# Kernel optimization log

Measured on AMD Instinct MI355X. Metric: run time of the kernel, lower is better.

Reference implementation:

```python
import jax, jax.numpy as jnp
import numpy as np
import math

C = 256
N_HEAD = 8
GROUPS = 32
EPS = 1e-5


def group_norm(x, scale, bias, groups=GROUPS, eps=EPS):
    # x: [B, C, H, W]
    b, c, h, w = x.shape
    xg = x.reshape(b, groups, c // groups, h, w)
    mean = xg.mean(axis=(2, 3, 4), keepdims=True)
    var = xg.var(axis=(2, 3, 4), keepdims=True)
    xg = (xg - mean) * jax.lax.rsqrt(var + eps)
    x = xg.reshape(b, c, h, w)
    return x * scale[None, :, None, None] + bias[None, :, None, None]


def setup_inputs() -> dict:
    key = jax.random.key(0)
    ks = jax.random.split(key, 8)
    B, H, W = 8, 32, 32
    inp = {
        "input_q": jax.random.normal(ks[0], (B, C, H, W), dtype=jnp.float32),
        "input_kv": jax.random.normal(ks[1], (B, C, H, W), dtype=jnp.float32),
        # GroupNorm affine params (torch default: weight=1, bias=0)
        "gq_scale": jnp.ones((C,), jnp.float32),
        "gq_bias": jnp.zeros((C,), jnp.float32),
        "gkv_scale": jnp.ones((C,), jnp.float32),
        "gkv_bias": jnp.zeros((C,), jnp.float32),
        # 1x1 convs as [out, in] matrices
        "Wq": jax.random.normal(ks[2], (C, C), dtype=jnp.float32) / math.sqrt(C),
        "Wkv": jax.random.normal(ks[3], (2 * C, C), dtype=jnp.float32) / math.sqrt(C),
        "Wout": jax.random.normal(ks[4], (C, C), dtype=jnp.float32) / math.sqrt(C),
        "bout": jnp.zeros((C,), jnp.float32),
    }
    return inp


def reference(input_q, input_kv, gq_scale, gq_bias, gkv_scale, gkv_bias, Wq, Wkv, Wout, bout):
    b, c, h, w = input_q.shape
    n = N_HEAD
    d = c // n

    norm_q = group_norm(input_q, gq_scale, gq_bias)
    query = jnp.einsum('oc,bchw->bohw', Wq, norm_q).reshape(b, n, d, h, w)

    norm_kv = group_norm(input_kv, gkv_scale, gkv_bias)
    kv = jnp.einsum('oc,bchw->bohw', Wkv, norm_kv).reshape(b, n, 2 * d, h, w)
    key, value = kv[:, :, :d], kv[:, :, d:]

    attn = jnp.einsum('bnchw,bncyx->bnhwyx', query, key) / math.sqrt(c)
    attn = jax.nn.softmax(attn.reshape(b, n, h, w, h * w), axis=-1)
    attn = attn.reshape(b, n, h, w, h, w)

    out = jnp.einsum('bnhwyx,bncyx->bnchw', attn, value).reshape(b, c, h, w)
    out = jnp.einsum('oc,bchw->bohw', Wout, out) + bout[None, :, None, None]
    return out + input_q
```

## Files before the change

### kernel.cpp

```cpp
#include <hip/hip_runtime.h>
#include <hip/hip_bf16.h>
#include <math.h>
#include <string.h>

#define NB 8
#define NC 256
#define HWSZ 1024
#define NHEAD 8
#define DHEAD 32
#define NGRP 32
#define CPG 8
#define EPSV 1e-5f

typedef float f32x4 __attribute__((ext_vector_type(4)));
typedef short bf16x8 __attribute__((ext_vector_type(8)));

__device__ __forceinline__ unsigned pk2(float a, float b) {
    __hip_bfloat162 h = __float22bfloat162_rn(make_float2(a, b));
    unsigned r;
    memcpy(&r, &h, sizeof(r));
    return r;
}
__device__ __forceinline__ unsigned pk2t(float a, float b) {
    unsigned ua = __float_as_uint(a), ub = __float_as_uint(b);
    return (ua >> 16) | (ub & 0xFFFF0000u);
}
__device__ __forceinline__ unsigned short f2bf(float x) {
    __hip_bfloat16 h = __float2bfloat16(x);
    unsigned short r;
    memcpy(&r, &h, sizeof(r));
    return r;
}
__device__ __forceinline__ float ex2(float x) { return __builtin_amdgcn_exp2f(x); }

__device__ __forceinline__ void gload_lds16(const void* g, void* l) {
    __builtin_amdgcn_global_load_lds(
        (const __attribute__((address_space(1))) unsigned int*)g,
        (__attribute__((address_space(3))) unsigned int*)l, 16, 0, 0);
}

__global__ void gn_stats_kernel(const float* __restrict__ xq,
                                const float* __restrict__ xkv,
                                float* __restrict__ stats) {
    int idx = blockIdx.x;
    int which = idx >> 8;
    int b = (idx >> 5) & 7;
    int g = idx & 31;
    const float* x = which ? xkv : xq;
    const float4* xb = (const float4*)(x + ((size_t)(b * NC + g * CPG)) * HWSZ);
    float s = 0.f, ss = 0.f;
    for (int i = threadIdx.x; i < (CPG * HWSZ) / 4; i += 256) {
        float4 v = xb[i];
        s += v.x + v.y + v.z + v.w;
        ss += v.x * v.x + v.y * v.y + v.z * v.z + v.w * v.w;
    }
    #pragma unroll
    for (int off = 32; off > 0; off >>= 1) {
        s += __shfl_down(s, off);
        ss += __shfl_down(ss, off);
    }
    __shared__ float red[8];
    int wid = threadIdx.x >> 6;
    if ((threadIdx.x & 63) == 0) { red[wid * 2] = s; red[wid * 2 + 1] = ss; }
    __syncthreads();
    if (threadIdx.x == 0) {
        float S = red[0] + red[2] + red[4] + red[6];
        float SS = red[1] + red[3] + red[5] + red[7];
        float mean = S * (1.f / (CPG * HWSZ));
        float var = SS * (1.f / (CPG * HWSZ)) - mean * mean;
        stats[idx * 2] = mean;
        stats[idx * 2 + 1] = rsqrtf(var + EPSV);
    }
}

__global__ void wconv_kernel(const float* __restrict__ Wq,
                             const float* __restrict__ Wkv,
                             const float* __restrict__ Wout,
                             unsigned short* __restrict__ wqb,
                             unsigned short* __restrict__ wkvb,
                             unsigned short* __restrict__ woutb) {
    int gid = blockIdx.x * 256 + threadIdx.x;
    int i0 = gid * 8;
    const float* src; unsigned short* dst; int off; float sc = 1.f;
    if (i0 < 65536)       { src = Wq;   dst = wqb;   off = i0;          sc = 0.0625f * 1.44269504088896f; }
    else if (i0 < 196608) { src = Wkv;  dst = wkvb;  off = i0 - 65536; }
    else                  { src = Wout; dst = woutb; off = i0 - 196608; }
    float4 v0 = *(const float4*)&src[off];
    float4 v1 = *(const float4*)&src[off + 4];
    uint4 o;
    o.x = pk2(v0.x * sc, v0.y * sc); o.y = pk2(v0.z * sc, v0.w * sc);
    o.z = pk2(v1.x * sc, v1.y * sc); o.w = pk2(v1.z * sc, v1.w * sc);
    *(uint4*)&dst[off] = o;
}

__global__ __launch_bounds__(256) void norm_t_kernel(
        const float* __restrict__ xq, const float* __restrict__ xkv,
        const float* __restrict__ stats,
        const float* __restrict__ sq, const float* __restrict__ bq,
        const float* __restrict__ skv, const float* __restrict__ bkv,
        unsigned short* __restrict__ xnq, unsigned short* __restrict__ xnkv) {
    __shared__ unsigned short T[64][72];
    const int bz = blockIdx.z;
    const int which = bz >> 3, b = bz & 7;
    const int c0 = blockIdx.y * 64, p0 = blockIdx.x * 64;
    const float* x  = which ? xkv : xq;
    const float* sc = which ? skv : sq;
    const float* bi = which ? bkv : bq;
    const float* st = stats + ((size_t)which * 256 + b * 32) * 2;
    const int tid = threadIdx.x;
    const int cb = tid >> 4, pb = tid & 15;
    float mm[4][4];
    #pragma unroll
    for (int u = 0; u < 4; ++u) {
        int c = c0 + cb * 4 + u;
        float4 v = *(const float4*)&x[((size_t)b * NC + c) * HWSZ + p0 + pb * 4];
        int gg = c >> 3;
        float mean = st[gg * 2], rstd = st[gg * 2 + 1];
        float a = rstd * sc[c];
        float bbv = bi[c] - mean * a;
        mm[u][0] = v.x * a + bbv; mm[u][1] = v.y * a + bbv;
        mm[u][2] = v.z * a + bbv; mm[u][3] = v.w * a + bbv;
    }
    #pragma unroll
    for (int v = 0; v < 4; ++v) {
        uint2 s2;
        s2.x = pk2(mm[0][v], mm[1][v]);
        s2.y = pk2(mm[2][v], mm[3][v]);
        *(uint2*)&T[pb * 4 + v][cb * 4] = s2;
    }
    __syncthreads();
    unsigned short* dst = (which ? xnkv : xnq) + (size_t)b * HWSZ * NC;
    #pragma unroll
    for (int it = 0; it < 2; ++it) {
        int i = tid + it * 256;
        int row = i >> 3, seg = i & 7;
        *(uint4*)&dst[(size_t)(p0 + row) * NC + c0 + seg * 8] = *(const uint4*)&T[row][seg * 8];
    }
}

template<int MODE>
__global__ __launch_bounds__(256) void gemm_kernel(
        const unsigned short* __restrict__ Abase,
        const unsigned short* __restrict__ Bbase,
        const float* __restrict__ bias_out,
        const float* __restrict__ resid,
        void* __restrict__ out0, void* __restrict__ out1) {
    __shared__ unsigned short As[64 * 256];
    __shared__ unsigned short Bs[64 * 256];
    const int tid = threadIdx.x;
    const int l16 = tid & 15, g = (tid >> 4) & 3, w = tid >> 6;
    const int o0 = blockIdx.y * 64;
    const size_t prow0 = (size_t)blockIdx.x * 64;
    const unsigned short* Asrc = (MODE < 2) ? (Abase + (size_t)o0 * NC) : (Abase + prow0 * NC);
    const unsigned short* Bsrc = (MODE < 2) ? (Bbase + prow0 * NC) : (Bbase + (size_t)o0 * NC);
    #pragma unroll
    for (int it = 0; it < 8; ++it) {
        int idx = tid + it * 256;
        int row = idx >> 5, seg = idx & 31;
        int ds = row * 256 + ((seg ^ (row & 7)) << 3);
        *(uint4*)&As[ds] = *(const uint4*)&Asrc[(size_t)row * NC + seg * 8];
        *(uint4*)&Bs[ds] = *(const uint4*)&Bsrc[(size_t)row * NC + seg * 8];
    }
    __syncthreads();
    f32x4 acc[4] = {};
    const int abase = (w * 16 + l16) * 256;
    const int asw = l16 & 7;
    #pragma unroll
    for (int kk = 0; kk < 8; ++kk) {
        const int koff = ((kk * 4 + g) ^ asw) << 3;
        bf16x8 a = *(const bf16x8*)&As[abase + koff];
        #pragma unroll
        for (int j = 0; j < 4; ++j) {
            bf16x8 b = *(const bf16x8*)&Bs[(j * 16 + l16) * 256 + koff];
            acc[j] = __builtin_amdgcn_mfma_f32_16x16x32_bf16(a, b, acc[j], 0, 0, 0);
        }
    }
    const int b = (int)(prow0 >> 10);
    const int pp = (int)(prow0 & 1023);
    if (MODE == 0) {
        int ob_ = o0 + 16 * w + 4 * g;
        int n = ob_ >> 5, d0 = ob_ & 31;
        unsigned short* dst = (unsigned short*)out0 + ((size_t)(b * NHEAD + n) * HWSZ) * DHEAD + d0;
        #pragma unroll
        for (int j = 0; j < 4; ++j) {
            int p = pp + 16 * j + l16;
            uint2 st;
            st.x = pk2(acc[j][0], acc[j][1]);
            st.y = pk2(acc[j][2], acc[j][3]);
            *(uint2*)&dst[(size_t)p * DHEAD] = st;
        }
    } else if (MODE == 1) {
        int n = o0 >> 6;
        int d0 = 16 * (w & 1) + 4 * g;
        if (w < 2) {
            unsigned short* dst = (unsigned short*)out0 + ((size_t)(b * NHEAD + n) * HWSZ) * DHEAD + d0;
            #pragma unroll
            for (int j = 0; j < 4; ++j) {
                int p = pp + 16 * j + l16;
                uint2 st;
                st.x = pk2(acc[j][0], acc[j][1]);
                st.y = pk2(acc[j][2], acc[j][3]);
                *(uint2*)&dst[(size_t)p * DHEAD] = st;
            }
        } else {
            unsigned short* dst = (unsigned short*)out1 + ((size_t)(b * NHEAD + n) * DHEAD + d0) * HWSZ;
            #pragma unroll
            for (int j = 0; j < 4; ++j) {
                int slot = ((l16 >> 2) << 3) + ((j & 1) << 2) + (l16 & 3);
                int p = pp + 32 * (j >> 1) + slot;
                #pragma unroll
                for (int r = 0; r < 4; ++r)
                    dst[(size_t)r * HWSZ + p] = f2bf(acc[j][r]);
            }
        }
    } else {
        int p_b = pp + 16 * w + 4 * g;
        #pragma unroll
        for (int j = 0; j < 4; ++j) {
            int o = o0 + 16 * j + l16;
            float bo = bias_out[o];
            size_t off = ((size_t)b * NC + o) * HWSZ + p_b;
            float4 rs = *(const float4*)&resid[off];
            float4 vst = make_float4(acc[j][0] + bo + rs.x, acc[j][1] + bo + rs.y,
                                     acc[j][2] + bo + rs.z, acc[j][3] + bo + rs.w);
            *(float4*)&((float*)out0)[off] = vst;
        }
    }
}

__global__ __launch_bounds__(256) void attn_mfma_kernel(
        const unsigned short* __restrict__ qb,
        const unsigned short* __restrict__ kb,
        const unsigned short* __restrict__ vb,
        unsigned short* __restrict__ ob) {
    __shared__ unsigned short KV[3][4096];
    const int tid = threadIdx.x;
    const int w = tid >> 6, lane = tid & 63;
    const int l16 = lane & 15, g = lane >> 4;
    const int F = blockIdx.y * 16 + blockIdx.x;
    const int bn = (F & 7) * 8 + (F >> 7);
    const int qblk = (F >> 3) & 15;
    const int qp = qblk * 64 + w * 16 + l16;

    bf16x8 qf = *(const bf16x8*)(qb + ((size_t)bn * HWSZ + qp) * DHEAD + g * 8);

    const int kr = tid >> 2, ks = tid & 3;
    const unsigned short* ksrc = kb + (size_t)bn * HWSZ * DHEAD
                               + (size_t)kr * DHEAD + ((ks ^ (kr & 3)) << 3);
    const int vr = tid >> 3, vs = tid & 7;
    const unsigned short* vsrc = vb + (size_t)bn * DHEAD * HWSZ
                               + (size_t)vr * HWSZ + ((vs ^ (vr & 7)) << 3);
    unsigned short* lk = &KV[0][0] + w * 512;
    unsigned short* lv = &KV[0][2048] + w * 512;

#define STAGE(t) do {                                                        \
        int b3_ = (t) % 3; int ti_ = (t) & 15;                               \
        gload_lds16(ksrc + (size_t)ti_ * 64 * DHEAD, lk + b3_ * 4096);       \
        gload_lds16(vsrc + (size_t)ti_ * 64,         lv + b3_ * 4096);       \
    } while (0)

    f32x4 acc0 = {0.f, 0.f, 0.f, 0.f}, acc1 = {0.f, 0.f, 0.f, 0.f};
    float m = -INFINITY, l0 = 0.f, l1 = 0.f;
    const f32x4 z = {0.f, 0.f, 0.f, 0.f};

    const int ksw  = (g ^ (l16 & 3)) << 3;
    const int vsw0 = ((g)     ^ (l16 & 7)) << 3;
    const int vsw1 = ((4 + g) ^ (l16 & 7)) << 3;

    STAGE(0);
    STAGE(1);

    for (int t = 0; t < 16; ++t) {
        const int cur = t % 3;
        asm volatile("s_waitcnt vmcnt(2)" ::: "memory");
        __builtin_amdgcn_s_barrier();
        STAGE(t + 2);

        const unsigned short* Kb = &KV[cur][0];
        const unsigned short* Vb = &KV[cur][2048];
        bf16x8 ka0 = *(const bf16x8*)&Kb[(l16)      * 32 + ksw];
        bf16x8 ka1 = *(const bf16x8*)&Kb[(16 + l16) * 32 + ksw];
        bf16x8 ka2 = *(const bf16x8*)&Kb[(32 + l16) * 32 + ksw];
        bf16x8 ka3 = *(const bf16x8*)&Kb[(48 + l16) * 32 + ksw];

        f32x4 s0 = __builtin_amdgcn_mfma_f32_16x16x32_bf16(ka0, qf, z, 0, 0, 0);
        f32x4 s1 = __builtin_amdgcn_mfma_f32_16x16x32_bf16(ka1, qf, z, 0, 0, 0);
        f32x4 s2 = __builtin_amdgcn_mfma_f32_16x16x32_bf16(ka2, qf, z, 0, 0, 0);
        f32x4 s3 = __builtin_amdgcn_mfma_f32_16x16x32_bf16(ka3, qf, z, 0, 0, 0);

        float ta = fmaxf(fmaxf(fmaxf(s0[0], s0[1]), fmaxf(s0[2], s0[3])),
                         fmaxf(fmaxf(s1[0], s1[1]), fmaxf(s1[2], s1[3])));
        float tb = fmaxf(fmaxf(fmaxf(s2[0], s2[1]), fmaxf(s2[2], s2[3])),
                         fmaxf(fmaxf(s3[0], s3[1]), fmaxf(s3[2], s3[3])));
        float tm = fmaxf(ta, tb);
        if (!__all(tm <= m + 8.f)) {
            float tmr = fmaxf(tm, __shfl_xor(tm, 16, 64));
            tmr = fmaxf(tmr, __shfl_xor(tmr, 32, 64));
            float mnew = fmaxf(m, tmr);
            float corr = ex2(m - mnew);
            acc0 *= corr; acc1 *= corr; l0 *= corr; l1 *= corr;
            m = mnew;
        }
        float p00 = ex2(s0[0] - m), p01 = ex2(s0[1] - m);
        float p02 = ex2(s0[2] - m), p03 = ex2(s0[3] - m);
        float p10 = ex2(s1[0] - m), p11 = ex2(s1[1] - m);
        float p12 = ex2(s1[2] - m), p13 = ex2(s1[3] - m);
        float p20 = ex2(s2[0] - m), p21 = ex2(s2[1] - m);
        float p22 = ex2(s2[2] - m), p23 = ex2(s2[3] - m);
        float p30 = ex2(s3[0] - m), p31 = ex2(s3[1] - m);
        float p32 = ex2(s3[2] - m), p33 = ex2(s3[3] - m);
        l0 += ((p00 + p01) + (p02 + p03)) + ((p10 + p11) + (p12 + p13));
        l1 += ((p20 + p21) + (p22 + p23)) + ((p30 + p31) + (p32 + p33));

        uint4 pwa, pwb;
        pwa.x = pk2t(p00, p01); pwa.y = pk2t(p02, p03);
        pwa.z = pk2t(p10, p11); pwa.w = pk2t(p12, p13);
        pwb.x = pk2t(p20, p21); pwb.y = pk2t(p22, p23);
        pwb.z = pk2t(p30, p31); pwb.w = pk2t(p32, p33);
        bf16x8 pf0, pf1;
        memcpy(&pf0, &pwa, sizeof(pf0));
        memcpy(&pf1, &pwb, sizeof(pf1));

        bf16x8 va0 = *(const bf16x8*)&Vb[(l16)      * 64 + vsw0];
        bf16x8 va1 = *(const bf16x8*)&Vb[(l16)      * 64 + vsw1];
        bf16x8 vb0 = *(const bf16x8*)&Vb[(16 + l16) * 64 + vsw0];
        bf16x8 vb1 = *(const bf16x8*)&Vb[(16 + l16) * 64 + vsw1];

        acc0 = __builtin_amdgcn_mfma_f32_16x16x32_bf16(va0, pf0, acc0, 0, 0, 0);
        acc0 = __builtin_amdgcn_mfma_f32_16x16x32_bf16(va1, pf1, acc0, 0, 0, 0);
        acc1 = __builtin_amdgcn_mfma_f32_16x16x32_bf16(vb0, pf0, acc1, 0, 0, 0);
        acc1 = __builtin_amdgcn_mfma_f32_16x16x32_bf16(vb1, pf1, acc1, 0, 0, 0);
    }
#undef STAGE

    float l = l0 + l1;
    l += __shfl_xor(l, 16, 64);
    l += __shfl_xor(l, 32, 64);
    float invl = 1.f / l;

    const int b = bn >> 3, n = bn & 7;
    unsigned short* dst = ob + ((size_t)b * HWSZ + qp) * NC + n * DHEAD;
    uint2 st0, st1;
    st0.x = pk2(acc0[0] * invl, acc0[1] * invl);
    st0.y = pk2(acc0[2] * invl, acc0[3] * invl);
    st1.x = pk2(acc1[0] * invl, acc1[1] * invl);
    st1.y = pk2(acc1[2] * invl, acc1[3] * invl);
    *(uint2*)&dst[4 * g]      = st0;
    *(uint2*)&dst[16 + 4 * g] = st1;
}

extern "C" void kernel_launch(void* const* d_in, const int* in_sizes, int n_in,
                              void* d_out, int out_size, void* d_ws, size_t ws_size,
                              hipStream_t stream) {
    const float* input_q  = (const float*)d_in[0];
    const float* input_kv = (const float*)d_in[1];
    const float* gq_scale = (const float*)d_in[2];
    const float* gq_bias  = (const float*)d_in[3];
    const float* gkv_scale = (const float*)d_in[4];
    const float* gkv_bias  = (const float*)d_in[5];
    const float* Wq   = (const float*)d_in[6];
    const float* Wkv  = (const float*)d_in[7];
    const float* Wout = (const float*)d_in[8];
    const float* bout = (const float*)d_in[9];
    float* out = (float*)d_out;

    char* ws = (char*)d_ws;
    float* stats = (float*)ws;
    unsigned short* wqb   = (unsigned short*)(ws + 16384);
    unsigned short* wkvb  = (unsigned short*)(ws + 16384 + 131072);
    unsigned short* woutb = (unsigned short*)(ws + 16384 + 131072 + 262144);
    const size_t MB = 1024 * 1024;
    unsigned short* xnq  = (unsigned short*)(ws + 1 * MB);
    unsigned short* xnkv = (unsigned short*)(ws + 5 * MB);
    unsigned short* qbuf = (unsigned short*)(ws + 9 * MB);
    unsigned short* kbuf = (unsigned short*)(ws + 13 * MB);
    unsigned short* vbuf = (unsigned short*)(ws + 17 * MB);
    unsigned short* obuf = (unsigned short*)(ws + 21 * MB);

    gn_stats_kernel<<<512, 256, 0, stream>>>(input_q, input_kv, stats);
    wconv_kernel<<<128, 256, 0, stream>>>(Wq, Wkv, Wout, wqb, wkvb, woutb);
    norm_t_kernel<<<dim3(16, 4, 16), 256, 0, stream>>>(
        input_q, input_kv, stats, gq_scale, gq_bias, gkv_scale, gkv_bias, xnq, xnkv);
    gemm_kernel<0><<<dim3(128, 4), 256, 0, stream>>>(wqb, xnq, nullptr, nullptr, qbuf, nullptr);
    gemm_kernel<1><<<dim3(128, 8), 256, 0, stream>>>(wkvb, xnkv, nullptr, nullptr, kbuf, vbuf);
    attn_mfma_kernel<<<dim3(16, 64), 256, 0, stream>>>(qbuf, kbuf, vbuf, obuf);
    gemm_kernel<2><<<dim3(128, 4), 256, 0, stream>>>(obuf, woutb, bout, input_q, out, nullptr);
}
```

Before: 55.01 us.

## Fuse group-norm apply into QKV GEMM and merge prep and QKV launches

Merges the GN-stats and weight-conversion kernels into one launch. Drops the separate normalize-transpose kernel: the QKV GEMM now reads fp32 input directly, applies the group-norm affine, and writes bf16 into swizzled LDS. Q and KV GEMMs are combined into one grid of 12 y-blocks. This removes the intermediate normalized-activation buffer round trip and three kernel launches. In exchange, each Q/KV output tile re-reads and re-normalizes the fp32 input redundantly (4 or 8 times per pixel block).

```diff
diff --git a/kernel.cpp b/kernel.cpp
--- a/kernel.cpp
+++ b/kernel.cpp
@@ -39,129 +39,127 @@
         (__attribute__((address_space(3))) unsigned int*)l, 16, 0, 0);
 }
 
-__global__ void gn_stats_kernel(const float* __restrict__ xq,
-                                const float* __restrict__ xkv,
-                                float* __restrict__ stats) {
-    int idx = blockIdx.x;
-    int which = idx >> 8;
-    int b = (idx >> 5) & 7;
-    int g = idx & 31;
-    const float* x = which ? xkv : xq;
-    const float4* xb = (const float4*)(x + ((size_t)(b * NC + g * CPG)) * HWSZ);
-    float s = 0.f, ss = 0.f;
-    for (int i = threadIdx.x; i < (CPG * HWSZ) / 4; i += 256) {
-        float4 v = xb[i];
-        s += v.x + v.y + v.z + v.w;
-        ss += v.x * v.x + v.y * v.y + v.z * v.z + v.w * v.w;
-    }
-    #pragma unroll
-    for (int off = 32; off > 0; off >>= 1) {
-        s += __shfl_down(s, off);
-        ss += __shfl_down(ss, off);
-    }
-    __shared__ float red[8];
-    int wid = threadIdx.x >> 6;
-    if ((threadIdx.x & 63) == 0) { red[wid * 2] = s; red[wid * 2 + 1] = ss; }
-    __syncthreads();
-    if (threadIdx.x == 0) {
-        float S = red[0] + red[2] + red[4] + red[6];
-        float SS = red[1] + red[3] + red[5] + red[7];
-        float mean = S * (1.f / (CPG * HWSZ));
-        float var = SS * (1.f / (CPG * HWSZ)) - mean * mean;
-        stats[idx * 2] = mean;
-        stats[idx * 2 + 1] = rsqrtf(var + EPSV);
-    }
-}
-
-__global__ void wconv_kernel(const float* __restrict__ Wq,
-                             const float* __restrict__ Wkv,
-                             const float* __restrict__ Wout,
-                             unsigned short* __restrict__ wqb,
-                             unsigned short* __restrict__ wkvb,
-                             unsigned short* __restrict__ woutb) {
-    int gid = blockIdx.x * 256 + threadIdx.x;
-    int i0 = gid * 8;
-    const float* src; unsigned short* dst; int off; float sc = 1.f;
-    if (i0 < 65536)       { src = Wq;   dst = wqb;   off = i0;          sc = 0.0625f * 1.44269504088896f; }
-    else if (i0 < 196608) { src = Wkv;  dst = wkvb;  off = i0 - 65536; }
-    else                  { src = Wout; dst = woutb; off = i0 - 196608; }
-    float4 v0 = *(const float4*)&src[off];
-    float4 v1 = *(const float4*)&src[off + 4];
-    uint4 o;
-    o.x = pk2(v0.x * sc, v0.y * sc); o.y = pk2(v0.z * sc, v0.w * sc);
-    o.z = pk2(v1.x * sc, v1.y * sc); o.w = pk2(v1.z * sc, v1.w * sc);
-    *(uint4*)&dst[off] = o;
-}
-
-__global__ __launch_bounds__(256) void norm_t_kernel(
+__global__ void prep_kernel(const float* __restrict__ xq,
+                            const float* __restrict__ xkv,
+                            float* __restrict__ stats,
+                            const float* __restrict__ Wq,
+                            const float* __restrict__ Wkv,
+                            const float* __restrict__ Wout,
+                            unsigned short* __restrict__ wqb,
+                            unsigned short* __restrict__ wkvb,
+                            unsigned short* __restrict__ woutb) {
+    if (blockIdx.x < 512) {
+        int idx = blockIdx.x;
+        int which = idx >> 8;
+        int b = (idx >> 5) & 7;
+        int g = idx & 31;
+        const float* x = which ? xkv : xq;
+        const float4* xb = (const float4*)(x + ((size_t)(b * NC + g * CPG)) * HWSZ);
+        float s = 0.f, ss = 0.f;
+        for (int i = threadIdx.x; i < (CPG * HWSZ) / 4; i += 256) {
+            float4 v = xb[i];
+            s += v.x + v.y + v.z + v.w;
+            ss += v.x * v.x + v.y * v.y + v.z * v.z + v.w * v.w;
+        }
+        #pragma unroll
+        for (int off = 32; off > 0; off >>= 1) {
+            s += __shfl_down(s, off);
+            ss += __shfl_down(ss, off);
+        }
+        __shared__ float red[8];
+        int wid = threadIdx.x >> 6;
+        if ((threadIdx.x & 63) == 0) { red[wid * 2] = s; red[wid * 2 + 1] = ss; }
+        __syncthreads();
+        if (threadIdx.x == 0) {
+            float S = red[0] + red[2] + red[4] + red[6];
+            float SS = red[1] + red[3] + red[5] + red[7];
+            float mean = S * (1.f / (CPG * HWSZ));
+            float var = SS * (1.f / (CPG * HWSZ)) - mean * mean;
+            stats[idx * 2] = mean;
+            stats[idx * 2 + 1] = rsqrtf(var + EPSV);
+        }
+    } else {
+        int gid = (blockIdx.x - 512) * 256 + threadIdx.x;
+        int i0 = gid * 8;
+        const float* src; unsigned short* dst; int off; float sc = 1.f;
+        if (i0 < 65536)       { src = Wq;   dst = wqb;   off = i0;          sc = 0.0625f * 1.44269504088896f; }
+        else if (i0 < 196608) { src = Wkv;  dst = wkvb;  off = i0 - 65536; }
+        else                  { src = Wout; dst = woutb; off = i0 - 196608; }
+        float4 v0 = *(const float4*)&src[off];
+        float4 v1 = *(const float4*)&src[off + 4];
+        uint4 o;
+        o.x = pk2(v0.x * sc, v0.y * sc); o.y = pk2(v0.z * sc, v0.w * sc);
+        o.z = pk2(v1.x * sc, v1.y * sc); o.w = pk2(v1.z * sc, v1.w * sc);
+        *(uint4*)&dst[off] = o;
+    }
+}
+
+__global__ __launch_bounds__(256) void qkv_gemm_kernel(
+        const unsigned short* __restrict__ wqb,
+        const unsigned short* __restrict__ wkvb,
         const float* __restrict__ xq, const float* __restrict__ xkv,
         const float* __restrict__ stats,
         const float* __restrict__ sq, const float* __restrict__ bq,
         const float* __restrict__ skv, const float* __restrict__ bkv,
-        unsigned short* __restrict__ xnq, unsigned short* __restrict__ xnkv) {
-    __shared__ unsigned short T[64][72];
-    const int bz = blockIdx.z;
-    const int which = bz >> 3, b = bz & 7;
-    const int c0 = blockIdx.y * 64, p0 = blockIdx.x * 64;
-    const float* x  = which ? xkv : xq;
-    const float* sc = which ? skv : sq;
-    const float* bi = which ? bkv : bq;
-    const float* st = stats + ((size_t)which * 256 + b * 32) * 2;
-    const int tid = threadIdx.x;
-    const int cb = tid >> 4, pb = tid & 15;
-    float mm[4][4];
-    #pragma unroll
-    for (int u = 0; u < 4; ++u) {
-        int c = c0 + cb * 4 + u;
-        float4 v = *(const float4*)&x[((size_t)b * NC + c) * HWSZ + p0 + pb * 4];
-        int gg = c >> 3;
-        float mean = st[gg * 2], rstd = st[gg * 2 + 1];
-        float a = rstd * sc[c];
-        float bbv = bi[c] - mean * a;
-        mm[u][0] = v.x * a + bbv; mm[u][1] = v.y * a + bbv;
-        mm[u][2] = v.z * a + bbv; mm[u][3] = v.w * a + bbv;
-    }
-    #pragma unroll
-    for (int v = 0; v < 4; ++v) {
-        uint2 s2;
-        s2.x = pk2(mm[0][v], mm[1][v]);
-        s2.y = pk2(mm[2][v], mm[3][v]);
-        *(uint2*)&T[pb * 4 + v][cb * 4] = s2;
-    }
-    __syncthreads();
-    unsigned short* dst = (which ? xnkv : xnq) + (size_t)b * HWSZ * NC;
-    #pragma unroll
-    for (int it = 0; it < 2; ++it) {
-        int i = tid + it * 256;
-        int row = i >> 3, seg = i & 7;
-        *(uint4*)&dst[(size_t)(p0 + row) * NC + c0 + seg * 8] = *(const uint4*)&T[row][seg * 8];
-    }
-}
-
-template<int MODE>
-__global__ __launch_bounds__(256) void gemm_kernel(
-        const unsigned short* __restrict__ Abase,
-        const unsigned short* __restrict__ Bbase,
-        const float* __restrict__ bias_out,
-        const float* __restrict__ resid,
-        void* __restrict__ out0, void* __restrict__ out1) {
+        unsigned short* __restrict__ qbuf,
+        unsigned short* __restrict__ kbuf,
+        unsigned short* __restrict__ vbuf) {
     __shared__ unsigned short As[64 * 256];
     __shared__ unsigned short Bs[64 * 256];
     const int tid = threadIdx.x;
     const int l16 = tid & 15, g = (tid >> 4) & 3, w = tid >> 6;
-    const int o0 = blockIdx.y * 64;
+    const int y = blockIdx.y;
+    const bool isQ = y < 4;
+    const int o0 = (isQ ? y : y - 4) * 64;
     const size_t prow0 = (size_t)blockIdx.x * 64;
-    const unsigned short* Asrc = (MODE < 2) ? (Abase + (size_t)o0 * NC) : (Abase + prow0 * NC);
-    const unsigned short* Bsrc = (MODE < 2) ? (Bbase + prow0 * NC) : (Bbase + (size_t)o0 * NC);
-    #pragma unroll
-    for (int it = 0; it < 8; ++it) {
+    const int b = (int)(prow0 >> 10);
+    const int pp = (int)(prow0 & 1023);
+
+    const unsigned short* Asrc = (isQ ? wqb : wkvb) + (size_t)o0 * NC;
+    const float* X  = (isQ ? xq : xkv) + (size_t)b * NC * HWSZ + pp;
+    const float* st = stats + (isQ ? 0 : 512) + b * 64;
+    const float* sc = isQ ? sq : skv;
+    const float* bi = isQ ? bq : bkv;
+
+    #pragma unroll
+    for (int it = 0; it < 2; ++it) {
         int idx = tid + it * 256;
-        int row = idx >> 5, seg = idx & 31;
-        int ds = row * 256 + ((seg ^ (row & 7)) << 3);
-        *(uint4*)&As[ds] = *(const uint4*)&Asrc[(size_t)row * NC + seg * 8];
-        *(uint4*)&Bs[ds] = *(const uint4*)&Bsrc[(size_t)row * NC + seg * 8];
+        int row = idx >> 3, seg2 = idx & 7;
+        #pragma unroll
+        for (int q4 = 0; q4 < 4; ++q4) {
+            int seg = seg2 * 4 + q4;
+            int ds = row * 256 + ((seg ^ (row & 7)) << 3);
+            *(uint4*)&As[ds] = *(const uint4*)&Asrc[(size_t)row * NC + seg * 8];
+        }
+    }
+    const int cq = tid >> 4, pq = tid & 15;
+    #pragma unroll
+    for (int j = 0; j < 4; ++j) {
+        int cb = cq * 4 + j * 64;
+        int grp = cb >> 3;
+        float mean = st[grp * 2], rstd = st[grp * 2 + 1];
+        float mm[4][4];
+        #pragma unroll
+        for (int u = 0; u < 4; ++u) {
+            int c = cb + u;
+            float4 v = *(const float4*)&X[(size_t)c * HWSZ + pq * 4];
+            float a = rstd * sc[c];
+            float bbv = bi[c] - mean * a;
+            mm[u][0] = v.x * a + bbv; mm[u][1] = v.y * a + bbv;
+            mm[u][2] = v.z * a + bbv; mm[u][3] = v.w * a + bbv;
+        }
+        #pragma unroll
+        for (int v2 = 0; v2 < 4; ++v2) {
+            int row = pq * 4 + v2;
+            int ds = row * 256 + ((((cb >> 3) ^ (row & 7))) << 3) + (cb & 7);
+            uint2 s2;
+            s2.x = pk2(mm[0][v2], mm[1][v2]);
+            s2.y = pk2(mm[2][v2], mm[3][v2]);
+            *(uint2*)&Bs[ds] = s2;
+        }
     }
     __syncthreads();
+
     f32x4 acc[4] = {};
     const int abase = (w * 16 + l16) * 256;
     const int asw = l16 & 7;
@@ -171,39 +169,38 @@
         bf16x8 a = *(const bf16x8*)&As[abase + koff];
         #pragma unroll
         for (int j = 0; j < 4; ++j) {
-            bf16x8 b = *(const bf16x8*)&Bs[(j * 16 + l16) * 256 + koff];
-            acc[j] = __builtin_amdgcn_mfma_f32_16x16x32_bf16(a, b, acc[j], 0, 0, 0);
-        }
-    }
-    const int b = (int)(prow0 >> 10);
-    const int pp = (int)(prow0 & 1023);
-    if (MODE == 0) {
+            bf16x8 bfr = *(const bf16x8*)&Bs[(j * 16 + l16) * 256 + koff];
+            acc[j] = __builtin_amdgcn_mfma_f32_16x16x32_bf16(a, bfr, acc[j], 0, 0, 0);
+        }
+    }
+
+    if (isQ) {
         int ob_ = o0 + 16 * w + 4 * g;
         int n = ob_ >> 5, d0 = ob_ & 31;
-        unsigned short* dst = (unsigned short*)out0 + ((size_t)(b * NHEAD + n) * HWSZ) * DHEAD + d0;
+        unsigned short* dst = qbuf + ((size_t)(b * NHEAD + n) * HWSZ) * DHEAD + d0;
         #pragma unroll
         for (int j = 0; j < 4; ++j) {
             int p = pp + 16 * j + l16;
-            uint2 st;
-            st.x = pk2(acc[j][0], acc[j][1]);
-            st.y = pk2(acc[j][2], acc[j][3]);
-            *(uint2*)&dst[(size_t)p * DHEAD] = st;
-        }
-    } else if (MODE == 1) {
+            uint2 st2;
+            st2.x = pk2(acc[j][0], acc[j][1]);
+            st2.y = pk2(acc[j][2], acc[j][3]);
+            *(uint2*)&dst[(size_t)p * DHEAD] = st2;
+        }
+    } else {
         int n = o0 >> 6;
         int d0 = 16 * (w & 1) + 4 * g;
         if (w < 2) {
-            unsigned short* dst = (unsigned short*)out0 + ((size_t)(b * NHEAD + n) * HWSZ) * DHEAD + d0;
+            unsigned short* dst = kbuf + ((size_t)(b * NHEAD + n) * HWSZ) * DHEAD + d0;
             #pragma unroll
             for (int j = 0; j < 4; ++j) {
                 int p = pp + 16 * j + l16;
-                uint2 st;
-                st.x = pk2(acc[j][0], acc[j][1]);
-                st.y = pk2(acc[j][2], acc[j][3]);
-                *(uint2*)&dst[(size_t)p * DHEAD] = st;
+                uint2 st2;
+                st2.x = pk2(acc[j][0], acc[j][1]);
+                st2.y = pk2(acc[j][2], acc[j][3]);
+                *(uint2*)&dst[(size_t)p * DHEAD] = st2;
             }
         } else {
-            unsigned short* dst = (unsigned short*)out1 + ((size_t)(b * NHEAD + n) * DHEAD + d0) * HWSZ;
+            unsigned short* dst = vbuf + ((size_t)(b * NHEAD + n) * DHEAD + d0) * HWSZ;
             #pragma unroll
             for (int j = 0; j < 4; ++j) {
                 int slot = ((l16 >> 2) << 3) + ((j & 1) << 2) + (l16 & 3);
@@ -213,18 +210,57 @@
                     dst[(size_t)r * HWSZ + p] = f2bf(acc[j][r]);
             }
         }
-    } else {
-        int p_b = pp + 16 * w + 4 * g;
+    }
+}
+
+__global__ __launch_bounds__(256) void out_gemm_kernel(
+        const unsigned short* __restrict__ Abase,
+        const unsigned short* __restrict__ Bbase,
+        const float* __restrict__ bias_out,
+        const float* __restrict__ resid,
+        float* __restrict__ out0) {
+    __shared__ unsigned short As[64 * 256];
+    __shared__ unsigned short Bs[64 * 256];
+    const int tid = threadIdx.x;
+    const int l16 = tid & 15, g = (tid >> 4) & 3, w = tid >> 6;
+    const int o0 = blockIdx.y * 64;
+    const size_t prow0 = (size_t)blockIdx.x * 64;
+    const unsigned short* Asrc = Abase + prow0 * NC;
+    const unsigned short* Bsrc = Bbase + (size_t)o0 * NC;
+    #pragma unroll
+    for (int it = 0; it < 8; ++it) {
+        int idx = tid + it * 256;
+        int row = idx >> 5, seg = idx & 31;
+        int ds = row * 256 + ((seg ^ (row & 7)) << 3);
+        *(uint4*)&As[ds] = *(const uint4*)&Asrc[(size_t)row * NC + seg * 8];
+        *(uint4*)&Bs[ds] = *(const uint4*)&Bsrc[(size_t)row * NC + seg * 8];
+    }
+    __syncthreads();
+    f32x4 acc[4] = {};
+    const int abase = (w * 16 + l16) * 256;
+    const int asw = l16 & 7;
+    #pragma unroll
+    for (int kk = 0; kk < 8; ++kk) {
+        const int koff = ((kk * 4 + g) ^ asw) << 3;
+        bf16x8 a = *(const bf16x8*)&As[abase + koff];
         #pragma unroll
         for (int j = 0; j < 4; ++j) {
-            int o = o0 + 16 * j + l16;
-            float bo = bias_out[o];
-            size_t off = ((size_t)b * NC + o) * HWSZ + p_b;
-            float4 rs = *(const float4*)&resid[off];
-            float4 vst = make_float4(acc[j][0] + bo + rs.x, acc[j][1] + bo + rs.y,
-                                     acc[j][2] + bo + rs.z, acc[j][3] + bo + rs.w);
-            *(float4*)&((float*)out0)[off] = vst;
-        }
+            bf16x8 b = *(const bf16x8*)&Bs[(j * 16 + l16) * 256 + koff];
+            acc[j] = __builtin_amdgcn_mfma_f32_16x16x32_bf16(a, b, acc[j], 0, 0, 0);
+        }
+    }
+    const int b = (int)(prow0 >> 10);
+    const int pp = (int)(prow0 & 1023);
+    int p_b = pp + 16 * w + 4 * g;
+    #pragma unroll
+    for (int j = 0; j < 4; ++j) {
+        int o = o0 + 16 * j + l16;
+        float bo = bias_out[o];
+        size_t off = ((size_t)b * NC + o) * HWSZ + p_b;
+        float4 rs = *(const float4*)&resid[off];
+        float4 vst = make_float4(acc[j][0] + bo + rs.x, acc[j][1] + bo + rs.y,
+                                 acc[j][2] + bo + rs.z, acc[j][3] + bo + rs.w);
+        *(float4*)&out0[off] = vst;
     }
 }
 
@@ -370,19 +406,16 @@
     unsigned short* wkvb  = (unsigned short*)(ws + 16384 + 131072);
     unsigned short* woutb = (unsigned short*)(ws + 16384 + 131072 + 262144);
     const size_t MB = 1024 * 1024;
-    unsigned short* xnq  = (unsigned short*)(ws + 1 * MB);
-    unsigned short* xnkv = (unsigned short*)(ws + 5 * MB);
-    unsigned short* qbuf = (unsigned short*)(ws + 9 * MB);
-    unsigned short* kbuf = (unsigned short*)(ws + 13 * MB);
-    unsigned short* vbuf = (unsigned short*)(ws + 17 * MB);
-    unsigned short* obuf = (unsigned short*)(ws + 21 * MB);
-
-    gn_stats_kernel<<<512, 256, 0, stream>>>(input_q, input_kv, stats);
-    wconv_kernel<<<128, 256, 0, stream>>>(Wq, Wkv, Wout, wqb, wkvb, woutb);
-    norm_t_kernel<<<dim3(16, 4, 16), 256, 0, stream>>>(
-        input_q, input_kv, stats, gq_scale, gq_bias, gkv_scale, gkv_bias, xnq, xnkv);
-    gemm_kernel<0><<<dim3(128, 4), 256, 0, stream>>>(wqb, xnq, nullptr, nullptr, qbuf, nullptr);
-    gemm_kernel<1><<<dim3(128, 8), 256, 0, stream>>>(wkvb, xnkv, nullptr, nullptr, kbuf, vbuf);
+    unsigned short* qbuf = (unsigned short*)(ws + 1 * MB);
+    unsigned short* kbuf = (unsigned short*)(ws + 5 * MB);
+    unsigned short* vbuf = (unsigned short*)(ws + 9 * MB);
+    unsigned short* obuf = (unsigned short*)(ws + 13 * MB);
+
+    prep_kernel<<<640, 256, 0, stream>>>(input_q, input_kv, stats,
+                                         Wq, Wkv, Wout, wqb, wkvb, woutb);
+    qkv_gemm_kernel<<<dim3(128, 12), 256, 0, stream>>>(
+        wqb, wkvb, input_q, input_kv, stats,
+        gq_scale, gq_bias, gkv_scale, gkv_bias, qbuf, kbuf, vbuf);
     attn_mfma_kernel<<<dim3(16, 64), 256, 0, stream>>>(qbuf, kbuf, vbuf, obuf);
-    gemm_kernel<2><<<dim3(128, 4), 256, 0, stream>>>(obuf, woutb, bout, input_q, out, nullptr);
-}
+    out_gemm_kernel<<<dim3(128, 4), 256, 0, stream>>>(obuf, woutb, bout, input_q, out);
+}
```

New measurement: 54.09 us. No clear change (-1.7%).
